# Performance work log

Hardware: AMD Instinct MI355X
Metric: run time of the kernel (lower is better)

## Reference

```python
import jax, jax.numpy as jnp
import numpy as np

DIM = 320
HEADS = 8
D_HEAD = 40
CTX_DIM = 768
INNER_FF = 4 * DIM  # 1280
EPS = 1e-5


def _ln(x, w, b):
    mu = jnp.mean(x, axis=-1, keepdims=True)
    var = jnp.mean(jnp.square(x - mu), axis=-1, keepdims=True)
    return (x - mu) * jax.lax.rsqrt(var + EPS) * w + b


def _attn(xq, ctx, Wq, Wk, Wv, Wo, bo):
    # Wq: [dim, inner]; Wk/Wv: [ctx_dim, inner]; Wo: [inner, dim]
    b, n, _ = xq.shape
    m = ctx.shape[1]
    scale = D_HEAD ** -0.5
    q = (xq @ Wq).reshape(b, n, HEADS, D_HEAD)
    k = (ctx @ Wk).reshape(b, m, HEADS, D_HEAD)
    v = (ctx @ Wv).reshape(b, m, HEADS, D_HEAD)
    sim = jnp.einsum('bihd,bjhd->bhij', q, k) * scale
    attn = jax.nn.softmax(sim, axis=-1)
    out = jnp.einsum('bhij,bjhd->bihd', attn, v).reshape(b, n, HEADS * D_HEAD)
    return out @ Wo + bo


def setup_inputs() -> dict:
    key = jax.random.key(0)
    ks = jax.random.split(key, 20)
    s = 0.02
    inner = HEADS * D_HEAD  # 320
    d = {
        'x': jax.random.normal(ks[0], (2, 4096, DIM), jnp.float32),
        'context': jax.random.normal(ks[1], (2, 77, CTX_DIM), jnp.float32),
        # norm params
        'ln1_w': jnp.ones((DIM,)), 'ln1_b': jnp.zeros((DIM,)),
        'ln2_w': jnp.ones((DIM,)), 'ln2_b': jnp.zeros((DIM,)),
        'ln3_w': jnp.ones((DIM,)), 'ln3_b': jnp.zeros((DIM,)),
        # attn1 (self)
        'a1_Wq': jax.random.normal(ks[2], (DIM, inner)) * s,
        'a1_Wk': jax.random.normal(ks[3], (DIM, inner)) * s,
        'a1_Wv': jax.random.normal(ks[4], (DIM, inner)) * s,
        'a1_Wo': jax.random.normal(ks[5], (inner, DIM)) * s,
        'a1_bo': jnp.zeros((DIM,)),
        # attn2 (cross)
        'a2_Wq': jax.random.normal(ks[6], (DIM, inner)) * s,
        'a2_Wk': jax.random.normal(ks[7], (CTX_DIM, inner)) * s,
        'a2_Wv': jax.random.normal(ks[8], (CTX_DIM, inner)) * s,
        'a2_Wo': jax.random.normal(ks[9], (inner, DIM)) * s,
        'a2_bo': jnp.zeros((DIM,)),
        # GEGLU feed-forward
        'ff_W1': jax.random.normal(ks[10], (DIM, 2 * INNER_FF)) * s,
        'ff_b1': jnp.zeros((2 * INNER_FF,)),
        'ff_W2': jax.random.normal(ks[11], (INNER_FF, DIM)) * s,
        'ff_b2': jnp.zeros((DIM,)),
    }
    return d


def reference(x, context, ln1_w, ln1_b, ln2_w, ln2_b, ln3_w, ln3_b,
              a1_Wq, a1_Wk, a1_Wv, a1_Wo, a1_bo,
              a2_Wq, a2_Wk, a2_Wv, a2_Wo, a2_bo,
              ff_W1, ff_b1, ff_W2, ff_b2):
    h = _ln(x, ln1_w, ln1_b)
    x = _attn(h, h, a1_Wq, a1_Wk, a1_Wv, a1_Wo, a1_bo) + x
    h = _ln(x, ln2_w, ln2_b)
    x = _attn(h, context, a2_Wq, a2_Wk, a2_Wv, a2_Wo, a2_bo) + x
    h = _ln(x, ln3_w, ln3_b)
    proj = h @ ff_W1 + ff_b1
    u, gate = jnp.split(proj, 2, axis=-1)
    ff = (u * jax.nn.gelu(gate, approximate=False)) @ ff_W2 + ff_b2
    return ff + x
```

## Files before the change

kernel.cpp:

```cpp
#include <hip/hip_runtime.h>
#include <hip/hip_bf16.h>
#include <math.h>

typedef __hip_bfloat16 bf16;
typedef __attribute__((ext_vector_type(8))) short bf16x8;
typedef __attribute__((ext_vector_type(4))) short bf16x4;
typedef __attribute__((ext_vector_type(4))) float f32x4;
typedef __attribute__((ext_vector_type(2))) unsigned int u32x2;

#define DIM 320
#define HEADS 8
#define DHEAD 40
#define CTXD 768
#define FFI 1280
#define NQ 4096
#define NCTX 77
#define BATCH 2

static __device__ __forceinline__ short f2bs(float v) {
    union { bf16 b; short s; } x; x.b = __float2bfloat16(v); return x.s;
}
static __device__ __forceinline__ float bs2f(short s) {
    return __uint_as_float(((unsigned)(unsigned short)s) << 16);
}
// ... 60 lines not shown
            for (int j = 0; j < 8; ++j) { v[j] = rp[j]; s += v[j]; s2 += v[j] * v[j]; }
        }
    }
#pragma unroll
    for (int off = 32; off; off >>= 1) { s += __shfl_xor(s, off); s2 += __shfl_xor(s2, off); }
    float mean = s * (1.f / DIM);
    float var = s2 * (1.f / DIM) - mean * mean;
    float rstd = rsqrtf(var + 1e-5f);
    if (lane < 40) {
        bf16x8 ov;
#pragma unroll
        for (int j = 0; j < 8; ++j)
            ov[j] = f2bs((v[j] - mean) * rstd * w[lane * 8 + j] + bp[lane * 8 + j]);
        *(bf16x8*)(out + (size_t)row * DIM + lane * 8) = ov;
    }
}

template<int MODE>
__global__ void __launch_bounds__(256) gemm128(const short* __restrict__ A,
                          const short* __restrict__ Wt,
                          const float* __restrict__ bias,
                          const float* __restrict__ res,
                          short* __restrict__ resb,
                          short* __restrict__ outb,
                          float* __restrict__ outf,
                          int N, int K, float oscale)
{
    __shared__ short As[128 * 72];
    __shared__ short Bs[64 * 72];
    const int tid = threadIdx.x;
    const int w = tid >> 6, lane = tid & 63, lrow = lane & 15, lgrp = lane >> 4;
    const int wr = w >> 1, wc = w & 1;
    const int m0 = blockIdx.y * 128, n0 = blockIdx.x * 64;
    f32x4 acc[4][2] = {};
    for (int k0 = 0; k0 < K; k0 += 64) {
        __syncthreads();
#pragma unroll
        for (int l = 0; l < 4; ++l) {
            int idx = tid + (l << 8);
            int arow = idx >> 3, ac = idx & 7;
            *(bf16x8*)&As[arow * 72 + ac * 8] =
                *(const bf16x8*)(A + (size_t)(m0 + arow) * K + k0 + ac * 8);
        }
#pragma unroll
        for (int l = 0; l < 2; ++l) {
            int idx = tid + (l << 8);
            int brow = idx >> 3, bc = idx & 7;
            *(bf16x8*)&Bs[brow * 72 + bc * 8] =
                *(const bf16x8*)(Wt + (size_t)(n0 + brow) * K + k0 + bc * 8);
        }
        __syncthreads();
#pragma unroll
        for (int s = 0; s < 2; ++s) {
            bf16x8 b0 = *(const bf16x8*)&Bs[(wc * 32 + lrow) * 72 + s * 32 + lgrp * 8];
            bf16x8 b1 = *(const bf16x8*)&Bs[(wc * 32 + 16 + lrow) * 72 + s * 32 + lgrp * 8];
#pragma unroll
            for (int m = 0; m < 4; ++m) {
                bf16x8 a = *(const bf16x8*)&As[(wr * 64 + m * 16 + lrow) * 72 + s * 32 + lgrp * 8];
                acc[m][0] = __builtin_amdgcn_mfma_f32_16x16x32_bf16(a, b0, acc[m][0], 0, 0, 0);
                acc[m][1] = __builtin_amdgcn_mfma_f32_16x16x32_bf16(a, b1, acc[m][1], 0, 0, 0);
            }
        }
    }
#pragma unroll
    for (int n = 0; n < 2; ++n) {
        int col = n0 + wc * 32 + n * 16 + lrow;
        float bvx = bias ? bias[col] : 0.f;
#pragma unroll
        for (int m = 0; m < 4; ++m) {
#pragma unroll
            for (int r = 0; r < 4; ++r) {
                int row = m0 + wr * 64 + m * 16 + lgrp * 4 + r;
                float v = acc[m][n][r] + bvx;
                size_t o = (size_t)row * N + col;
                if (MODE == 0)      outb[o] = f2bs(v * oscale);
                else if (MODE == 1) resb[o] = f2bs(v + res[o]);
                else if (MODE == 2) resb[o] = f2bs(v + bs2f(resb[o]));
                else                outf[o] = v + bs2f(resb[o]);
            }
        }
    }
}

__global__ void __launch_bounds__(256) qkv128(const short* __restrict__ A,
                          const short* __restrict__ wq, const short* __restrict__ wk,
                          const short* __restrict__ wv,
                          short* __restrict__ qb, short* __restrict__ kbuf,
                          short* __restrict__ vts, float qscale)
{
    __shared__ short As[128 * 72];
    __shared__ short Bs[64 * 72];
    const int tid = threadIdx.x;
    const int z = blockIdx.z;
    const short* Wt = z == 0 ? wq : z == 1 ? wk : wv;
    const int w = tid >> 6, lane = tid & 63, lrow = lane & 15, lgrp = lane >> 4;
    const int wr = w >> 1, wc = w & 1;
    const int m0 = blockIdx.y * 128, n0 = blockIdx.x * 64;
    f32x4 acc[4][2] = {};
    for (int k0 = 0; k0 < DIM; k0 += 64) {
        __syncthreads();
#pragma unroll
        for (int l = 0; l < 4; ++l) {
            int idx = tid + (l << 8);
            int arow = idx >> 3, ac = idx & 7;
            *(bf16x8*)&As[arow * 72 + ac * 8] =
                *(const bf16x8*)(A + (size_t)(m0 + arow) * DIM + k0 + ac * 8);
        }
#pragma unroll
        for (int l = 0; l < 2; ++l) {
            int idx = tid + (l << 8);
            int brow = idx >> 3, bc = idx & 7;
            *(bf16x8*)&Bs[brow * 72 + bc * 8] =
                *(const bf16x8*)(Wt + (size_t)(n0 + brow) * DIM + k0 + bc * 8);
        }
        __syncthreads();
#pragma unroll
        for (int s = 0; s < 2; ++s) {
            bf16x8 b0 = *(const bf16x8*)&Bs[(wc * 32 + lrow) * 72 + s * 32 + lgrp * 8];
            bf16x8 b1 = *(const bf16x8*)&Bs[(wc * 32 + 16 + lrow) * 72 + s * 32 + lgrp * 8];
#pragma unroll
            for (int m = 0; m < 4; ++m) {
                bf16x8 a = *(const bf16x8*)&As[(wr * 64 + m * 16 + lrow) * 72 + s * 32 + lgrp * 8];
                acc[m][0] = __builtin_amdgcn_mfma_f32_16x16x32_bf16(a, b0, acc[m][0], 0, 0, 0);
                acc[m][1] = __builtin_amdgcn_mfma_f32_16x16x32_bf16(a, b1, acc[m][1], 0, 0, 0);
            }
        }
    }
#pragma unroll
    for (int n = 0; n < 2; ++n) {
        int col = n0 + wc * 32 + n * 16 + lrow;
#pragma unroll
        for (int m = 0; m < 4; ++m) {
            if (z == 2) {
                int row0 = m0 + wr * 64 + m * 16 + lgrp * 4;
                int b_ = row0 >> 12, kv = row0 & (NQ - 1);
                int hh = col / DHEAD, d = col - hh * DHEAD;
                bf16x4 pv;
#pragma unroll
                for (int r = 0; r < 4; ++r) pv[r] = f2bs(acc[m][n][r]);
                *(bf16x4*)(vts + (size_t)((b_ * HEADS + hh) * 48 + d) * NQ + kv) = pv;
            } else {
#pragma unroll
                for (int r = 0; r < 4; ++r) {
                    int row = m0 + wr * 64 + m * 16 + lgrp * 4 + r;
                    float v = acc[m][n][r];
                    if (z == 0) qb[(size_t)row * DIM + col] = f2bs(v * qscale);
                    else        kbuf[(size_t)row * DIM + col] = f2bs(v);
                }
            }
        }
    }
}

__global__ void __launch_bounds__(256) geglu128(const short* __restrict__ A,
                           const short* __restrict__ Wt1,
                           const float* __restrict__ b1, short* __restrict__ G)
{
    __shared__ short As[128 * 72];
    __shared__ short Bu[64 * 72];
    __shared__ short Bg[64 * 72];
    const int tid = threadIdx.x;
    const int w = tid >> 6, lane = tid & 63, lrow = lane & 15, lgrp = lane >> 4;
    const int wr = w >> 1, wc = w & 1;
    const int m0 = blockIdx.y * 128, n0 = blockIdx.x * 64;
    f32x4 au[4][2] = {}, ag[4][2] = {};
    for (int k0 = 0; k0 < DIM; k0 += 64) {
        __syncthreads();
#pragma unroll
        for (int l = 0; l < 4; ++l) {
            int idx = tid + (l << 8);
            int arow = idx >> 3, ac = idx & 7;
            *(bf16x8*)&As[arow * 72 + ac * 8] =
                *(const bf16x8*)(A + (size_t)(m0 + arow) * DIM + k0 + ac * 8);
        }
#pragma unroll
        for (int l = 0; l < 2; ++l) {
            int idx = tid + (l << 8);
            int brow = idx >> 3, bc = idx & 7;
            *(bf16x8*)&Bu[brow * 72 + bc * 8] =
                *(const bf16x8*)(Wt1 + (size_t)(n0 + brow) * DIM + k0 + bc * 8);
            *(bf16x8*)&Bg[brow * 72 + bc * 8] =
                *(const bf16x8*)(Wt1 + (size_t)(FFI + n0 + brow) * DIM + k0 + bc * 8);
        }
        __syncthreads();
#pragma unroll
        for (int s = 0; s < 2; ++s) {
            bf16x8 bu0 = *(const bf16x8*)&Bu[(wc * 32 + lrow) * 72 + s * 32 + lgrp * 8];
            bf16x8 bu1 = *(const bf16x8*)&Bu[(wc * 32 + 16 + lrow) * 72 + s * 32 + lgrp * 8];
            bf16x8 bg0 = *(const bf16x8*)&Bg[(wc * 32 + lrow) * 72 + s * 32 + lgrp * 8];
            bf16x8 bg1 = *(const bf16x8*)&Bg[(wc * 32 + 16 + lrow) * 72 + s * 32 + lgrp * 8];
#pragma unroll
            for (int m = 0; m < 4; ++m) {
                bf16x8 a = *(const bf16x8*)&As[(wr * 64 + m * 16 + lrow) * 72 + s * 32 + lgrp * 8];
                au[m][0] = __builtin_amdgcn_mfma_f32_16x16x32_bf16(a, bu0, au[m][0], 0, 0, 0);
                au[m][1] = __builtin_amdgcn_mfma_f32_16x16x32_bf16(a, bu1, au[m][1], 0, 0, 0);
                ag[m][0] = __builtin_amdgcn_mfma_f32_16x16x32_bf16(a, bg0, ag[m][0], 0, 0, 0);
                ag[m][1] = __builtin_amdgcn_mfma_f32_16x16x32_bf16(a, bg1, ag[m][1], 0, 0, 0);
            }
        }
    }
#pragma unroll
    for (int n = 0; n < 2; ++n) {
        int col = n0 + wc * 32 + n * 16 + lrow;
        float bu = b1[col], bg = b1[FFI + col];
#pragma unroll
        for (int m = 0; m < 4; ++m) {
#pragma unroll
            for (int r = 0; r < 4; ++r) {
                int row = m0 + wr * 64 + m * 16 + lgrp * 4 + r;
                float u = au[m][n][r] + bu;
                float g = ag[m][n][r] + bg;
                float gelu = 0.5f * g * (1.f + erff(g * 0.70710678f));
                G[(size_t)row * FFI + col] = f2bs(u * gelu);
            }
        }
    }
}

__global__ void __launch_bounds__(256) mfma_crosskv(const float* __restrict__ ctx,
                          const short* __restrict__ wk2, const short* __restrict__ wv2,
                          short* __restrict__ k2, short* __restrict__ vt2)
{
    __shared__ short As[64 * 72];
    __shared__ short Bs[64 * 72];
    const int tid = threadIdx.x;
    const int z = blockIdx.z;
    const short* Wt = z ? wv2 : wk2;
    const int Mc = BATCH * NCTX;
    const int w = tid >> 6, lane = tid & 63, lrow = lane & 15, lgrp = lane >> 4;
    const int m0 = blockIdx.y * 64, n0 = blockIdx.x * 64;
    f32x4 acc[4] = {};
    for (int kb = 0; kb < CTXD / 64; ++kb) {
        const int k0 = kb << 6;
        __syncthreads();
#pragma unroll
        for (int l = 0; l < 2; ++l) {
            int idx = tid + (l << 8);
            int arow = idx >> 3, ac = idx & 7;
            int grow = m0 + arow;
            bf16x8 v = {};
            if (grow < Mc) {
                const float* Af = ctx + (size_t)grow * CTXD + k0 + ac * 8;
#pragma unroll
                for (int j = 0; j < 8; ++j) v[j] = f2bs(Af[j]);
            }
            *(bf16x8*)&As[arow * 72 + ac * 8] = v;
            *(bf16x8*)&Bs[arow * 72 + ac * 8] =
                *(const bf16x8*)(Wt + (size_t)(n0 + arow) * CTXD + k0 + ac * 8);
        }
        __syncthreads();
#pragma unroll
        for (int s = 0; s < 2; ++s) {
            bf16x8 a = *(const bf16x8*)&As[(w * 16 + lrow) * 72 + s * 32 + lgrp * 8];
#pragma unroll
            for (int ct = 0; ct < 4; ++ct) {
                bf16x8 b = *(const bf16x8*)&Bs[(ct * 16 + lrow) * 72 + s * 32 + lgrp * 8];
                acc[ct] = __builtin_amdgcn_mfma_f32_16x16x32_bf16(a, b, acc[ct], 0, 0, 0);
            }
        }
    }
#pragma unroll
    for (int ct = 0; ct < 4; ++ct) {
        int col = n0 + ct * 16 + lrow;
#pragma unroll
        for (int r = 0; r < 4; ++r) {
            int row = m0 + w * 16 + lgrp * 4 + r;
            if (row >= Mc) continue;
            float v = acc[ct][r];
            if (z == 0) k2[(size_t)row * DIM + col] = f2bs(v);
            else {
                int b_ = row / NCTX, kv = row - b_ * NCTX;
                int hh = col / DHEAD, d = col - hh * DHEAD;
                vt2[(size_t)((b_ * HEADS + hh) * 48 + d) * 128 + kv] = f2bs(v);
            }
        }
    }
}

template<bool FULL>
__global__ void __launch_bounds__(256) flash_mfma(const short* __restrict__ Q,
                           const short* __restrict__ Kb,
                           const short* __restrict__ VtG,
                           short* __restrict__ O,
                           int kvlen, int kvs)
{
    __shared__ short Ks[2][64 * 64];
    __shared__ short Vt[2][48 * 64];
    __shared__ short Ps[128 * 64];
    const int tid = threadIdx.x;
    const int w = tid >> 6, lane = tid & 63, lrow = lane & 15, lgrp = lane >> 4;
    const int hh = blockIdx.y, b = blockIdx.z;
    const int q0 = blockIdx.x * 128;
    const int swz = (lrow & 7) << 4;

    for (int i = tid; i < 1024; i += 256) ((bf16x8*)Ks)[i] = (bf16x8){};
    for (int i = tid; i < 768; i += 256) {
        short fill = (((i % 384) >> 3) == 40) ? (short)0x3F80 : (short)0;
        bf16x8 f8 = {fill, fill, fill, fill, fill, fill, fill, fill};
        ((bf16x8*)Vt)[i] = f8;
    }

    const size_t qra = (size_t)(b * NQ + q0 + w * 32 + lrow) * DIM + hh * DHEAD;
    const size_t qrb = qra + (size_t)16 * DIM;
    bf16x8 bq0a = *(const bf16x8*)(Q + qra + lgrp * 8);
    bf16x8 bq0b = *(const bf16x8*)(Q + qrb + lgrp * 8);
    bf16x8 bq1a = {}, bq1b = {};
    if (lgrp == 0) {
        bq1a = *(const bf16x8*)(Q + qra + 32);
        bq1b = *(const bf16x8*)(Q + qrb + 32);
    }

    const int kv0 = tid / 5, cc0 = tid % 5;
    const bool isK1 = tid < 64;
    const int kv1 = (256 + tid) / 5, cc1 = (256 + tid) % 5;
    const int vd1 = (tid - 64) >> 3, vcc1 = (tid - 64) & 7;
    const bool hasV2 = tid < 128;
    const int vd2 = (192 + tid) >> 3, vcc2 = (192 + tid) & 7;

    bf16x8 st0, st1, st2;
    const size_t kbase = (size_t)b * kvlen;
    const size_t vbase = (size_t)((b * HEADS + hh) * 48);

    auto issue = [&](int t) {
        const int j0 = t << 6;
        st0 = *(const bf16x8*)(Kb + (kbase + j0 + kv0) * DIM + hh * DHEAD + cc0 * 8);
        if (isK1) st1 = *(const bf16x8*)(Kb + (kbase + j0 + kv1) * DIM + hh * DHEAD + cc1 * 8);
        else      st1 = *(const bf16x8*)(VtG + (vbase + vd1) * kvs + j0 + vcc1 * 8);
        if (hasV2) st2 = *(const bf16x8*)(VtG + (vbase + vd2) * kvs + j0 + vcc2 * 8);
    };
    auto commit = [&](int bi) {
        *(bf16x8*)((char*)Ks[bi] + kv0 * 128 + ((cc0 * 16) ^ ((kv0 & 7) << 4))) = st0;
        if (isK1)
            *(bf16x8*)((char*)Ks[bi] + kv1 * 128 + ((cc1 * 16) ^ ((kv1 & 7) << 4))) = st1;
        else
            *(bf16x8*)((char*)Vt[bi] + vd1 * 128 + ((vcc1 * 16) ^ ((vd1 & 7) << 4))) = st1;
        if (hasV2)
            *(bf16x8*)((char*)Vt[bi] + vd2 * 128 + ((vcc2 * 16) ^ ((vd2 & 7) << 4))) = st2;
    };

    f32x4 oa[3] = {}, ob[3] = {};

    issue(0);
    __syncthreads();
    commit(0);
    const int ntiles = (kvlen + 63) >> 6;
    char* prow_a = (char*)Ps + (w * 32 + lrow) * 128;
    char* prow_b = prow_a + 16 * 128;
    for (int t = 0; t < ntiles; ++t) {
        const int j0 = t << 6;
        const int bi = t & 1;
        if (t + 1 < ntiles) issue(t + 1);
        __syncthreads();

        f32x4 sa[4] = {}, sb[4] = {};
        __builtin_amdgcn_s_setprio(1);
#pragma unroll
        for (int ct = 0; ct < 4; ++ct) {
            const char* krow = (char*)Ks[bi] + (ct * 16 + lrow) * 128;
            bf16x8 ak0 = *(const bf16x8*)(krow + ((lgrp * 16) ^ swz));
            bf16x8 ak1 = *(const bf16x8*)(krow + ((64 + lgrp * 16) ^ swz));
            sa[ct] = __builtin_amdgcn_mfma_f32_16x16x32_bf16(ak0, bq0a, sa[ct], 0, 0, 0);
            sb[ct] = __builtin_amdgcn_mfma_f32_16x16x32_bf16(ak0, bq0b, sb[ct], 0, 0, 0);
            sa[ct] = __builtin_amdgcn_mfma_f32_16x16x32_bf16(ak1, bq1a, sa[ct], 0, 0, 0);
            sb[ct] = __builtin_amdgcn_mfma_f32_16x16x32_bf16(ak1, bq1b, sb[ct], 0, 0, 0);
        }
        __builtin_amdgcn_s_setprio(0);
        if (!FULL && j0 + 64 > kvlen) {
#pragma unroll
            for (int ct = 0; ct < 4; ++ct)
#pragma unroll
                for (int r = 0; r < 4; ++r)
                    if (j0 + ct * 16 + lgrp * 4 + r >= kvlen) { sa[ct][r] = -1e30f; sb[ct][r] = -1e30f; }
        }
#pragma unroll
        for (int ct = 0; ct < 4; ++ct) {
            float a0 = __builtin_amdgcn_exp2f(sa[ct][0]);
            float a1 = __builtin_amdgcn_exp2f(sa[ct][1]);
            float a2 = __builtin_amdgcn_exp2f(sa[ct][2]);
            float a3 = __builtin_amdgcn_exp2f(sa[ct][3]);
            u32x2 pka; pka[0] = pkbf(a1, a0); pka[1] = pkbf(a3, a2);
            *(u32x2*)(prow_a + ((ct * 32 + lgrp * 8) ^ swz)) = pka;
            float b0 = __builtin_amdgcn_exp2f(sb[ct][0]);
            float b1 = __builtin_amdgcn_exp2f(sb[ct][1]);
            float b2 = __builtin_amdgcn_exp2f(sb[ct][2]);
            float b3 = __builtin_amdgcn_exp2f(sb[ct][3]);
            u32x2 pkb; pkb[0] = pkbf(b1, b0); pkb[1] = pkbf(b3, b2);
            *(u32x2*)(prow_b + ((ct * 32 + lgrp * 8) ^ swz)) = pkb;
        }
        __builtin_amdgcn_s_setprio(1);
#pragma unroll
        for (int s = 0; s < 2; ++s) {
            bf16x8 bpa = *(const bf16x8*)(prow_a + ((s * 64 + lgrp * 16) ^ swz));
            bf16x8 bpb = *(const bf16x8*)(prow_b + ((s * 64 + lgrp * 16) ^ swz));
#pragma unroll
            for (int dt = 0; dt < 3; ++dt) {
                bf16x8 av = *(const bf16x8*)((char*)Vt[bi] + (dt * 16 + lrow) * 128 + ((s * 64 + lgrp * 16) ^ swz));
                oa[dt] = __builtin_amdgcn_mfma_f32_16x16x32_bf16(av, bpa, oa[dt], 0, 0, 0);
                ob[dt] = __builtin_amdgcn_mfma_f32_16x16x32_bf16(av, bpb, ob[dt], 0, 0, 0);
            }
        }
        __builtin_amdgcn_s_setprio(0);
        if (t + 1 < ntiles) commit((t + 1) & 1);
    }
    float la = __shfl(oa[2][0], 32 + lrow);
    float lb = __shfl(ob[2][0], 32 + lrow);
    float ia = 1.f / la, ib = 1.f / lb;
#pragma unroll
    for (int dt = 0; dt < 3; ++dt) {
        int dbase = dt * 16 + lgrp * 4;
        if (dbase < DHEAD) {
            u32x2 ova, ovb;
            ova[0] = pkbf(oa[dt][1] * ia, oa[dt][0] * ia);
            ova[1] = pkbf(oa[dt][3] * ia, oa[dt][2] * ia);
            *(u32x2*)(O + qra + dbase) = ova;
            ovb[0] = pkbf(ob[dt][1] * ib, ob[dt][0] * ib);
            ovb[1] = pkbf(ob[dt][3] * ib, ob[dt][2] * ib);
            *(u32x2*)(O + qrb + dbase) = ovb;
        }
    }
}

extern "C" void kernel_launch(void* const* d_in, const int* in_sizes, int n_in,
                              void* d_out, int out_size, void* d_ws, size_t ws_size,
                              hipStream_t stream)
{
    const float* x      = (const float*)d_in[0];
    const float* ctx    = (const float*)d_in[1];
    const float* ln1_w  = (const float*)d_in[2];
    const float* ln1_b  = (const float*)d_in[3];
    const float* ln2_w  = (const float*)d_in[4];
    const float* ln2_b  = (const float*)d_in[5];
    const float* ln3_w  = (const float*)d_in[6];
    const float* ln3_b  = (const float*)d_in[7];
    const float* a1_Wq  = (const float*)d_in[8];
    const float* a1_Wk  = (const float*)d_in[9];
    const float* a1_Wv  = (const float*)d_in[10];
    const float* a1_Wo  = (const float*)d_in[11];
    const float* a1_bo  = (const float*)d_in[12];
    const float* a2_Wq  = (const float*)d_in[13];
    const float* a2_Wk  = (const float*)d_in[14];
    const float* a2_Wv  = (const float*)d_in[15];
    const float* a2_Wo  = (const float*)d_in[16];
    const float* a2_bo  = (const float*)d_in[17];
    const float* ff_W1  = (const float*)d_in[18];
    const float* ff_b1  = (const float*)d_in[19];
    const float* ff_W2  = (const float*)d_in[20];
    const float* ff_b2  = (const float*)d_in[21];

    const int M = BATCH * NQ;
    const float qscale2 = (float)(0.15811388300841898 * 1.4426950408889634);

    char* p = (char*)d_ws;
    auto carve = [&](size_t bytes) { char* r = p; p += (bytes + 255) & ~255ULL; return r; };
    short* h       = (short*)carve((size_t)M * DIM * 2);
    short* qb      = (short*)carve((size_t)M * DIM * 2);
    short* kbuf    = (short*)carve((size_t)M * DIM * 2);
    short* attnout = (short*)carve((size_t)M * DIM * 2);
    short* resb    = (short*)carve((size_t)M * DIM * 2);
    short* gbuf    = (short*)carve((size_t)M * FFI * 2);
    short* VtS     = (short*)carve((size_t)BATCH * HEADS * 48 * NQ * 2);
    short* Vt2     = (short*)carve((size_t)BATCH * HEADS * 48 * 128 * 2);
    short* k2      = (short*)carve((size_t)256 * DIM * 2);
    short* wtq1    = (short*)carve((size_t)DIM * DIM * 2);
    short* wtk1    = (short*)carve((size_t)DIM * DIM * 2);
    short* wtv1    = (short*)carve((size_t)DIM * DIM * 2);
    short* wto1    = (short*)carve((size_t)DIM * DIM * 2);
    short* wtq2    = (short*)carve((size_t)DIM * DIM * 2);
    short* wto2    = (short*)carve((size_t)DIM * DIM * 2);
    short* wtk2    = (short*)carve((size_t)DIM * CTXD * 2);
    short* wtv2    = (short*)carve((size_t)DIM * CTXD * 2);
    short* wt1     = (short*)carve((size_t)2 * FFI * DIM * 2);
    short* wt2     = (short*)carve((size_t)DIM * FFI * 2);

    dim3 blk(256);
    dim3 g128(DIM / 64, M / 128);
    dim3 gattn(NQ / 128, HEADS, BATCH);

    wtrans_all<<<2280, blk, 0, stream>>>(a1_Wq, a1_Wk, a1_Wv, a1_Wo, a2_Wq, a2_Wo,
                                         a2_Wk, a2_Wv, ff_W1, ff_W2,
                                         wtq1, wtk1, wtv1, wto1, wtq2, wto2,
                                         wtk2, wtv2, wt1, wt2);
    ln_kernel<false><<<M / 4, blk, 0, stream>>>(x, ln1_w, ln1_b, h, M);
    qkv128<<<dim3(5, 64, 3), blk, 0, stream>>>(h, wtq1, wtk1, wtv1, qb, kbuf, VtS, qscale2);
    flash_mfma<true><<<gattn, blk, 0, stream>>>(qb, kbuf, VtS, attnout, NQ, NQ);
    gemm128<1><<<g128, blk, 0, stream>>>(attnout, wto1, a1_bo, x, resb, nullptr, nullptr, DIM, DIM, 1.f);
    ln_kernel<true><<<M / 4, blk, 0, stream>>>(resb, ln2_w, ln2_b, h, M);
    gemm128<0><<<g128, blk, 0, stream>>>(h, wtq2, nullptr, nullptr, nullptr, qb, nullptr, DIM, DIM, qscale2);
    mfma_crosskv<<<dim3(5, 3, 2), blk, 0, stream>>>(ctx, wtk2, wtv2, k2, Vt2);
    flash_mfma<false><<<gattn, blk, 0, stream>>>(qb, k2, Vt2, attnout, NCTX, 128);
    gemm128<2><<<g128, blk, 0, stream>>>(attnout, wto2, a2_bo, nullptr, resb, nullptr, nullptr, DIM, DIM, 1.f);
    ln_kernel<true><<<M / 4, blk, 0, stream>>>(resb, ln3_w, ln3_b, h, M);
    geglu128<<<dim3(FFI / 64, M / 128), blk, 0, stream>>>(h, wt1, ff_b1, gbuf);
    gemm128<3><<<g128, blk, 0, stream>>>(gbuf, wt2, ff_b2, nullptr, resb, nullptr, (float*)d_out, DIM, FFI, 1.f);
}
```

Measured before the change: 233.9 us.

## Fuse Q/K/V and cross K/V projections; restructure flash attention prefetch loop

The self-attention QKV projection now computes Q, K and V in one block that shares the loaded activation tile, instead of three grid slices that each reload it. The cross-attention K/V projection is fused the same way. The flash attention loop is unrolled by two with fixed double-buffer indices, precomputed swizzled shared-memory offsets and incremented global pointers, and it now commits the prefetched tile at the top of each iteration. In exchange, the QKV kernel holds three times the accumulators and launches a third as many blocks, which may lower occupancy. The prefetch also reads past the end of the K/V data, so the k2 buffer is enlarged to absorb those over-reads.

```diff
diff --git a/kernel.cpp b/kernel.cpp
--- a/kernel.cpp
+++ b/kernel.cpp
@@ -166,21 +166,21 @@
     }
 }
 
-__global__ void __launch_bounds__(256) qkv128(const short* __restrict__ A,
+__global__ void __launch_bounds__(256) qkv_fused(const short* __restrict__ A,
                           const short* __restrict__ wq, const short* __restrict__ wk,
                           const short* __restrict__ wv,
                           short* __restrict__ qb, short* __restrict__ kbuf,
                           short* __restrict__ vts, float qscale)
 {
     __shared__ short As[128 * 72];
-    __shared__ short Bs[64 * 72];
+    __shared__ short Bq[64 * 72];
+    __shared__ short Bk[64 * 72];
+    __shared__ short Bv[64 * 72];
     const int tid = threadIdx.x;
-    const int z = blockIdx.z;
-    const short* Wt = z == 0 ? wq : z == 1 ? wk : wv;
     const int w = tid >> 6, lane = tid & 63, lrow = lane & 15, lgrp = lane >> 4;
     const int wr = w >> 1, wc = w & 1;
     const int m0 = blockIdx.y * 128, n0 = blockIdx.x * 64;
-    f32x4 acc[4][2] = {};
+    f32x4 aq[4][2] = {}, ak[4][2] = {}, av[4][2] = {};
     for (int k0 = 0; k0 < DIM; k0 += 64) {
         __syncthreads();
 #pragma unroll
@@ -194,44 +194,109 @@
         for (int l = 0; l < 2; ++l) {
             int idx = tid + (l << 8);
             int brow = idx >> 3, bc = idx & 7;
-            *(bf16x8*)&Bs[brow * 72 + bc * 8] =
-                *(const bf16x8*)(Wt + (size_t)(n0 + brow) * DIM + k0 + bc * 8);
+            size_t wo = (size_t)(n0 + brow) * DIM + k0 + bc * 8;
+            *(bf16x8*)&Bq[brow * 72 + bc * 8] = *(const bf16x8*)(wq + wo);
+            *(bf16x8*)&Bk[brow * 72 + bc * 8] = *(const bf16x8*)(wk + wo);
+            *(bf16x8*)&Bv[brow * 72 + bc * 8] = *(const bf16x8*)(wv + wo);
         }
         __syncthreads();
 #pragma unroll
         for (int s = 0; s < 2; ++s) {
-            bf16x8 b0 = *(const bf16x8*)&Bs[(wc * 32 + lrow) * 72 + s * 32 + lgrp * 8];
-            bf16x8 b1 = *(const bf16x8*)&Bs[(wc * 32 + 16 + lrow) * 72 + s * 32 + lgrp * 8];
+            int bo0 = (wc * 32 + lrow) * 72 + s * 32 + lgrp * 8;
+            int bo1 = bo0 + 16 * 72;
+            bf16x8 q0 = *(const bf16x8*)&Bq[bo0], q1 = *(const bf16x8*)&Bq[bo1];
+            bf16x8 kk0 = *(const bf16x8*)&Bk[bo0], kk1 = *(const bf16x8*)&Bk[bo1];
+            bf16x8 v0 = *(const bf16x8*)&Bv[bo0], v1 = *(const bf16x8*)&Bv[bo1];
 #pragma unroll
             for (int m = 0; m < 4; ++m) {
                 bf16x8 a = *(const bf16x8*)&As[(wr * 64 + m * 16 + lrow) * 72 + s * 32 + lgrp * 8];
-                acc[m][0] = __builtin_amdgcn_mfma_f32_16x16x32_bf16(a, b0, acc[m][0], 0, 0, 0);
-                acc[m][1] = __builtin_amdgcn_mfma_f32_16x16x32_bf16(a, b1, acc[m][1], 0, 0, 0);
+                aq[m][0] = __builtin_amdgcn_mfma_f32_16x16x32_bf16(a, q0, aq[m][0], 0, 0, 0);
+                aq[m][1] = __builtin_amdgcn_mfma_f32_16x16x32_bf16(a, q1, aq[m][1], 0, 0, 0);
+                ak[m][0] = __builtin_amdgcn_mfma_f32_16x16x32_bf16(a, kk0, ak[m][0], 0, 0, 0);
+                ak[m][1] = __builtin_amdgcn_mfma_f32_16x16x32_bf16(a, kk1, ak[m][1], 0, 0, 0);
+                av[m][0] = __builtin_amdgcn_mfma_f32_16x16x32_bf16(a, v0, av[m][0], 0, 0, 0);
+                av[m][1] = __builtin_amdgcn_mfma_f32_16x16x32_bf16(a, v1, av[m][1], 0, 0, 0);
             }
         }
     }
 #pragma unroll
     for (int n = 0; n < 2; ++n) {
         int col = n0 + wc * 32 + n * 16 + lrow;
+        int hh = col / DHEAD, d = col - hh * DHEAD;
 #pragma unroll
         for (int m = 0; m < 4; ++m) {
-            if (z == 2) {
-                int row0 = m0 + wr * 64 + m * 16 + lgrp * 4;
-                int b_ = row0 >> 12, kv = row0 & (NQ - 1);
-                int hh = col / DHEAD, d = col - hh * DHEAD;
-                bf16x4 pv;
-#pragma unroll
-                for (int r = 0; r < 4; ++r) pv[r] = f2bs(acc[m][n][r]);
-                *(bf16x4*)(vts + (size_t)((b_ * HEADS + hh) * 48 + d) * NQ + kv) = pv;
-            } else {
-#pragma unroll
-                for (int r = 0; r < 4; ++r) {
-                    int row = m0 + wr * 64 + m * 16 + lgrp * 4 + r;
-                    float v = acc[m][n][r];
-                    if (z == 0) qb[(size_t)row * DIM + col] = f2bs(v * qscale);
-                    else        kbuf[(size_t)row * DIM + col] = f2bs(v);
-                }
-            }
+            int row0 = m0 + wr * 64 + m * 16 + lgrp * 4;
+            int b_ = row0 >> 12, kv = row0 & (NQ - 1);
+            bf16x4 pv;
+#pragma unroll
+            for (int r = 0; r < 4; ++r) pv[r] = f2bs(av[m][n][r]);
+            *(bf16x4*)(vts + (size_t)((b_ * HEADS + hh) * 48 + d) * NQ + kv) = pv;
+#pragma unroll
+            for (int r = 0; r < 4; ++r) {
+                int row = row0 + r;
+                qb[(size_t)row * DIM + col] = f2bs(aq[m][n][r] * qscale);
+                kbuf[(size_t)row * DIM + col] = f2bs(ak[m][n][r]);
+            }
+        }
+    }
+}
+
+__global__ void __launch_bounds__(256) crosskv_fused(const float* __restrict__ ctx,
+                          const short* __restrict__ wk2, const short* __restrict__ wv2,
+                          short* __restrict__ k2, short* __restrict__ vt2)
+{
+    __shared__ short As[64 * 72];
+    __shared__ short Bk[64 * 72];
+    __shared__ short Bv[64 * 72];
+    const int tid = threadIdx.x;
+    const int Mc = BATCH * NCTX;
+    const int w = tid >> 6, lane = tid & 63, lrow = lane & 15, lgrp = lane >> 4;
+    const int m0 = blockIdx.y * 64, n0 = blockIdx.x * 64;
+    f32x4 acck[4] = {}, accv[4] = {};
+    for (int kb = 0; kb < CTXD / 64; ++kb) {
+        const int k0 = kb << 6;
+        __syncthreads();
+#pragma unroll
+        for (int l = 0; l < 2; ++l) {
+            int idx = tid + (l << 8);
+            int arow = idx >> 3, ac = idx & 7;
+            int grow = m0 + arow;
+            bf16x8 v = {};
+            if (grow < Mc) {
+                const float* Af = ctx + (size_t)grow * CTXD + k0 + ac * 8;
+#pragma unroll
+                for (int j = 0; j < 8; ++j) v[j] = f2bs(Af[j]);
+            }
+            *(bf16x8*)&As[arow * 72 + ac * 8] = v;
+            size_t wo = (size_t)(n0 + arow) * CTXD + k0 + ac * 8;
+            *(bf16x8*)&Bk[arow * 72 + ac * 8] = *(const bf16x8*)(wk2 + wo);
+            *(bf16x8*)&Bv[arow * 72 + ac * 8] = *(const bf16x8*)(wv2 + wo);
+        }
+        __syncthreads();
+#pragma unroll
+        for (int s = 0; s < 2; ++s) {
+            bf16x8 a = *(const bf16x8*)&As[(w * 16 + lrow) * 72 + s * 32 + lgrp * 8];
+#pragma unroll
+            for (int ct = 0; ct < 4; ++ct) {
+                int bo = (ct * 16 + lrow) * 72 + s * 32 + lgrp * 8;
+                bf16x8 bk = *(const bf16x8*)&Bk[bo];
+                acck[ct] = __builtin_amdgcn_mfma_f32_16x16x32_bf16(a, bk, acck[ct], 0, 0, 0);
+                bf16x8 bv = *(const bf16x8*)&Bv[bo];
+                accv[ct] = __builtin_amdgcn_mfma_f32_16x16x32_bf16(a, bv, accv[ct], 0, 0, 0);
+            }
+        }
+    }
+#pragma unroll
+    for (int ct = 0; ct < 4; ++ct) {
+        int col = n0 + ct * 16 + lrow;
+        int hh = col / DHEAD, d = col - hh * DHEAD;
+#pragma unroll
+        for (int r = 0; r < 4; ++r) {
+            int row = m0 + w * 16 + lgrp * 4 + r;
+            if (row >= Mc) continue;
+            k2[(size_t)row * DIM + col] = f2bs(acck[ct][r]);
+            int b_ = row / NCTX, kv = row - b_ * NCTX;
+            vt2[(size_t)((b_ * HEADS + hh) * 48 + d) * 128 + kv] = f2bs(accv[ct][r]);
         }
     }
 }
@@ -301,66 +366,6 @@
     }
 }
 
-__global__ void __launch_bounds__(256) mfma_crosskv(const float* __restrict__ ctx,
-                          const short* __restrict__ wk2, const short* __restrict__ wv2,
-                          short* __restrict__ k2, short* __restrict__ vt2)
-{
-    __shared__ short As[64 * 72];
-    __shared__ short Bs[64 * 72];
-    const int tid = threadIdx.x;
-    const int z = blockIdx.z;
-    const short* Wt = z ? wv2 : wk2;
-    const int Mc = BATCH * NCTX;
-    const int w = tid >> 6, lane = tid & 63, lrow = lane & 15, lgrp = lane >> 4;
-    const int m0 = blockIdx.y * 64, n0 = blockIdx.x * 64;
-    f32x4 acc[4] = {};
-    for (int kb = 0; kb < CTXD / 64; ++kb) {
-        const int k0 = kb << 6;
-        __syncthreads();
-#pragma unroll
-        for (int l = 0; l < 2; ++l) {
-            int idx = tid + (l << 8);
-            int arow = idx >> 3, ac = idx & 7;
-            int grow = m0 + arow;
-            bf16x8 v = {};
-            if (grow < Mc) {
-                const float* Af = ctx + (size_t)grow * CTXD + k0 + ac * 8;
-#pragma unroll
-                for (int j = 0; j < 8; ++j) v[j] = f2bs(Af[j]);
-            }
-            *(bf16x8*)&As[arow * 72 + ac * 8] = v;
-            *(bf16x8*)&Bs[arow * 72 + ac * 8] =
-                *(const bf16x8*)(Wt + (size_t)(n0 + arow) * CTXD + k0 + ac * 8);
-        }
-        __syncthreads();
-#pragma unroll
-        for (int s = 0; s < 2; ++s) {
-            bf16x8 a = *(const bf16x8*)&As[(w * 16 + lrow) * 72 + s * 32 + lgrp * 8];
-#pragma unroll
-            for (int ct = 0; ct < 4; ++ct) {
-                bf16x8 b = *(const bf16x8*)&Bs[(ct * 16 + lrow) * 72 + s * 32 + lgrp * 8];
-                acc[ct] = __builtin_amdgcn_mfma_f32_16x16x32_bf16(a, b, acc[ct], 0, 0, 0);
-            }
-        }
-    }
-#pragma unroll
-    for (int ct = 0; ct < 4; ++ct) {
-        int col = n0 + ct * 16 + lrow;
-#pragma unroll
-        for (int r = 0; r < 4; ++r) {
-            int row = m0 + w * 16 + lgrp * 4 + r;
-            if (row >= Mc) continue;
-            float v = acc[ct][r];
-            if (z == 0) k2[(size_t)row * DIM + col] = f2bs(v);
-            else {
-                int b_ = row / NCTX, kv = row - b_ * NCTX;
-                int hh = col / DHEAD, d = col - hh * DHEAD;
-                vt2[(size_t)((b_ * HEADS + hh) * 48 + d) * 128 + kv] = f2bs(v);
-            }
-        }
-    }
-}
-
 template<bool FULL>
 __global__ void __launch_bounds__(256) flash_mfma(const short* __restrict__ Q,
                            const short* __restrict__ Kb,
@@ -401,40 +406,41 @@
     const bool hasV2 = tid < 128;
     const int vd2 = (192 + tid) >> 3, vcc2 = (192 + tid) & 7;
 
-    bf16x8 st0, st1, st2;
     const size_t kbase = (size_t)b * kvlen;
     const size_t vbase = (size_t)((b * HEADS + hh) * 48);
 
-    auto issue = [&](int t) {
-        const int j0 = t << 6;
-        st0 = *(const bf16x8*)(Kb + (kbase + j0 + kv0) * DIM + hh * DHEAD + cc0 * 8);
-        if (isK1) st1 = *(const bf16x8*)(Kb + (kbase + j0 + kv1) * DIM + hh * DHEAD + cc1 * 8);
-        else      st1 = *(const bf16x8*)(VtG + (vbase + vd1) * kvs + j0 + vcc1 * 8);
-        if (hasV2) st2 = *(const bf16x8*)(VtG + (vbase + vd2) * kvs + j0 + vcc2 * 8);
+    const short* kp0 = Kb + (kbase + kv0) * DIM + hh * DHEAD + cc0 * 8;
+    const short* kp1 = Kb + (kbase + (isK1 ? kv1 : 0)) * DIM + hh * DHEAD + (isK1 ? cc1 : 0) * 8;
+    const short* vp1 = VtG + (vbase + (isK1 ? 0 : vd1)) * kvs + (isK1 ? 0 : vcc1) * 8;
+    const short* vp2 = VtG + (vbase + (hasV2 ? vd2 : 0)) * kvs + (hasV2 ? vcc2 : 0) * 8;
+
+    const int koff0 = kv0 * 128 + ((cc0 * 16) ^ ((kv0 & 7) << 4));
+    const int koff1 = kv1 * 128 + ((cc1 * 16) ^ ((kv1 & 7) << 4));
+    const int voff1 = vd1 * 128 + ((vcc1 * 16) ^ ((vd1 & 7) << 4));
+    const int voff2 = vd2 * 128 + ((vcc2 * 16) ^ ((vd2 & 7) << 4));
+
+    bf16x8 st0, st1, st2;
+    auto issue = [&]() {
+        st0 = *(const bf16x8*)kp0; kp0 += 64 * DIM;
+        if (isK1) { st1 = *(const bf16x8*)kp1; kp1 += 64 * DIM; }
+        else      { st1 = *(const bf16x8*)vp1; vp1 += 64; }
+        if (hasV2) { st2 = *(const bf16x8*)vp2; vp2 += 64; }
     };
     auto commit = [&](int bi) {
-        *(bf16x8*)((char*)Ks[bi] + kv0 * 128 + ((cc0 * 16) ^ ((kv0 & 7) << 4))) = st0;
-        if (isK1)
-            *(bf16x8*)((char*)Ks[bi] + kv1 * 128 + ((cc1 * 16) ^ ((kv1 & 7) << 4))) = st1;
-        else
-            *(bf16x8*)((char*)Vt[bi] + vd1 * 128 + ((vcc1 * 16) ^ ((vd1 & 7) << 4))) = st1;
-        if (hasV2)
-            *(bf16x8*)((char*)Vt[bi] + vd2 * 128 + ((vcc2 * 16) ^ ((vd2 & 7) << 4))) = st2;
+        *(bf16x8*)((char*)Ks[bi] + koff0) = st0;
+        if (isK1)  *(bf16x8*)((char*)Ks[bi] + koff1) = st1;
+        else       *(bf16x8*)((char*)Vt[bi] + voff1) = st1;
+        if (hasV2) *(bf16x8*)((char*)Vt[bi] + voff2) = st2;
     };
 
     f32x4 oa[3] = {}, ob[3] = {};
-
-    issue(0);
-    __syncthreads();
-    commit(0);
-    const int ntiles = (kvlen + 63) >> 6;
     char* prow_a = (char*)Ps + (w * 32 + lrow) * 128;
     char* prow_b = prow_a + 16 * 128;
-    for (int t = 0; t < ntiles; ++t) {
-        const int j0 = t << 6;
-        const int bi = t & 1;
-        if (t + 1 < ntiles) issue(t + 1);
-        __syncthreads();
+
+    auto body = [&](int t, int bi) {
+        __syncthreads();
+        commit(bi ^ 1);
+        issue();
 
         f32x4 sa[4] = {}, sb[4] = {};
         __builtin_amdgcn_s_setprio(1);
@@ -449,12 +455,12 @@
             sb[ct] = __builtin_amdgcn_mfma_f32_16x16x32_bf16(ak1, bq1b, sb[ct], 0, 0, 0);
         }
         __builtin_amdgcn_s_setprio(0);
-        if (!FULL && j0 + 64 > kvlen) {
+        if (!FULL && (t << 6) + 64 > kvlen) {
 #pragma unroll
             for (int ct = 0; ct < 4; ++ct)
 #pragma unroll
                 for (int r = 0; r < 4; ++r)
-                    if (j0 + ct * 16 + lgrp * 4 + r >= kvlen) { sa[ct][r] = -1e30f; sb[ct][r] = -1e30f; }
+                    if ((t << 6) + ct * 16 + lgrp * 4 + r >= kvlen) { sa[ct][r] = -1e30f; sb[ct][r] = -1e30f; }
         }
 #pragma unroll
         for (int ct = 0; ct < 4; ++ct) {
@@ -484,8 +490,18 @@
             }
         }
         __builtin_amdgcn_s_setprio(0);
-        if (t + 1 < ntiles) commit((t + 1) & 1);
-    }
+    };
+
+    issue();
+    __syncthreads();
+    commit(0);
+    issue();
+    const int ntiles = (kvlen + 63) >> 6;
+    for (int t = 0; t < ntiles; t += 2) {
+        body(t, 0);
+        body(t + 1, 1);
+    }
+
     float la = __shfl(oa[2][0], 32 + lrow);
     float lb = __shfl(ob[2][0], 32 + lrow);
     float ia = 1.f / la, ib = 1.f / lb;
@@ -544,7 +560,7 @@
     short* gbuf    = (short*)carve((size_t)M * FFI * 2);
     short* VtS     = (short*)carve((size_t)BATCH * HEADS * 48 * NQ * 2);
     short* Vt2     = (short*)carve((size_t)BATCH * HEADS * 48 * 128 * 2);
-    short* k2      = (short*)carve((size_t)256 * DIM * 2);
+    short* k2      = (short*)carve((size_t)512 * DIM * 2);
     short* wtq1    = (short*)carve((size_t)DIM * DIM * 2);
     short* wtk1    = (short*)carve((size_t)DIM * DIM * 2);
     short* wtv1    = (short*)carve((size_t)DIM * DIM * 2);
@@ -565,12 +581,12 @@
                                          wtq1, wtk1, wtv1, wto1, wtq2, wto2,
                                          wtk2, wtv2, wt1, wt2);
     ln_kernel<false><<<M / 4, blk, 0, stream>>>(x, ln1_w, ln1_b, h, M);
-    qkv128<<<dim3(5, 64, 3), blk, 0, stream>>>(h, wtq1, wtk1, wtv1, qb, kbuf, VtS, qscale2);
+    qkv_fused<<<g128, blk, 0, stream>>>(h, wtq1, wtk1, wtv1, qb, kbuf, VtS, qscale2);
     flash_mfma<true><<<gattn, blk, 0, stream>>>(qb, kbuf, VtS, attnout, NQ, NQ);
     gemm128<1><<<g128, blk, 0, stream>>>(attnout, wto1, a1_bo, x, resb, nullptr, nullptr, DIM, DIM, 1.f);
     ln_kernel<true><<<M / 4, blk, 0, stream>>>(resb, ln2_w, ln2_b, h, M);
     gemm128<0><<<g128, blk, 0, stream>>>(h, wtq2, nullptr, nullptr, nullptr, qb, nullptr, DIM, DIM, qscale2);
-    mfma_crosskv<<<dim3(5, 3, 2), blk, 0, stream>>>(ctx, wtk2, wtv2, k2, Vt2);
+    crosskv_fused<<<dim3(5, 3), blk, 0, stream>>>(ctx, wtk2, wtv2, k2, Vt2);
     flash_mfma<false><<<gattn, blk, 0, stream>>>(qb, k2, Vt2, attnout, NCTX, 128);
     gemm128<2><<<g128, blk, 0, stream>>>(attnout, wto2, a2_bo, nullptr, resb, nullptr, nullptr, DIM, DIM, 1.f);
     ln_kernel<true><<<M / 4, blk, 0, stream>>>(resb, ln3_w, ln3_b, h, M);
```

Measured after the change: 244.4 us. 1.04x slower.

## Software-pipeline flash attention: defer PV matmul one tile and triple-buffer V

Applied to the files above, without the earlier changes.

Restructures the flash attention loop so the P·V MFMA for tile t-1 runs while tile t's QK scores and exponentials are computed. P gets double buffers and V triple buffers so the next tile's global-to-LDS commit can happen right after the barrier. Global load pointers and LDS offsets are precomputed and advanced incrementally, and prefetching now runs two tiles ahead, which over-reads past kvlen (hence the enlarged k2 buffer). The cost is more LDS per block, which may lower occupancy, and one extra drain step after the loop.

```diff
diff --git a/kernel.cpp b/kernel.cpp
--- a/kernel.cpp
+++ b/kernel.cpp
@@ -236,71 +236,6 @@
     }
 }
 
-__global__ void __launch_bounds__(256) geglu128(const short* __restrict__ A,
-                           const short* __restrict__ Wt1,
-                           const float* __restrict__ b1, short* __restrict__ G)
-{
-    __shared__ short As[128 * 72];
-    __shared__ short Bu[64 * 72];
-    __shared__ short Bg[64 * 72];
-    const int tid = threadIdx.x;
-    const int w = tid >> 6, lane = tid & 63, lrow = lane & 15, lgrp = lane >> 4;
-    const int wr = w >> 1, wc = w & 1;
-    const int m0 = blockIdx.y * 128, n0 = blockIdx.x * 64;
-    f32x4 au[4][2] = {}, ag[4][2] = {};
-    for (int k0 = 0; k0 < DIM; k0 += 64) {
-        __syncthreads();
-#pragma unroll
-        for (int l = 0; l < 4; ++l) {
-            int idx = tid + (l << 8);
-            int arow = idx >> 3, ac = idx & 7;
-            *(bf16x8*)&As[arow * 72 + ac * 8] =
-                *(const bf16x8*)(A + (size_t)(m0 + arow) * DIM + k0 + ac * 8);
-        }
-#pragma unroll
-        for (int l = 0; l < 2; ++l) {
-            int idx = tid + (l << 8);
-            int brow = idx >> 3, bc = idx & 7;
-            *(bf16x8*)&Bu[brow * 72 + bc * 8] =
-                *(const bf16x8*)(Wt1 + (size_t)(n0 + brow) * DIM + k0 + bc * 8);
-            *(bf16x8*)&Bg[brow * 72 + bc * 8] =
-                *(const bf16x8*)(Wt1 + (size_t)(FFI + n0 + brow) * DIM + k0 + bc * 8);
-        }
-        __syncthreads();
-#pragma unroll
-        for (int s = 0; s < 2; ++s) {
-            bf16x8 bu0 = *(const bf16x8*)&Bu[(wc * 32 + lrow) * 72 + s * 32 + lgrp * 8];
-            bf16x8 bu1 = *(const bf16x8*)&Bu[(wc * 32 + 16 + lrow) * 72 + s * 32 + lgrp * 8];
-            bf16x8 bg0 = *(const bf16x8*)&Bg[(wc * 32 + lrow) * 72 + s * 32 + lgrp * 8];
-            bf16x8 bg1 = *(const bf16x8*)&Bg[(wc * 32 + 16 + lrow) * 72 + s * 32 + lgrp * 8];
-#pragma unroll
-            for (int m = 0; m < 4; ++m) {
-                bf16x8 a = *(const bf16x8*)&As[(wr * 64 + m * 16 + lrow) * 72 + s * 32 + lgrp * 8];
-                au[m][0] = __builtin_amdgcn_mfma_f32_16x16x32_bf16(a, bu0, au[m][0], 0, 0, 0);
-                au[m][1] = __builtin_amdgcn_mfma_f32_16x16x32_bf16(a, bu1, au[m][1], 0, 0, 0);
-                ag[m][0] = __builtin_amdgcn_mfma_f32_16x16x32_bf16(a, bg0, ag[m][0], 0, 0, 0);
-                ag[m][1] = __builtin_amdgcn_mfma_f32_16x16x32_bf16(a, bg1, ag[m][1], 0, 0, 0);
-            }
-        }
-    }
-#pragma unroll
-    for (int n = 0; n < 2; ++n) {
-        int col = n0 + wc * 32 + n * 16 + lrow;
-        float bu = b1[col], bg = b1[FFI + col];
-#pragma unroll
-        for (int m = 0; m < 4; ++m) {
-#pragma unroll
-            for (int r = 0; r < 4; ++r) {
-                int row = m0 + wr * 64 + m * 16 + lgrp * 4 + r;
-                float u = au[m][n][r] + bu;
-                float g = ag[m][n][r] + bg;
-                float gelu = 0.5f * g * (1.f + erff(g * 0.70710678f));
-                G[(size_t)row * FFI + col] = f2bs(u * gelu);
-            }
-        }
-    }
-}
-
 __global__ void __launch_bounds__(256) mfma_crosskv(const float* __restrict__ ctx,
                           const short* __restrict__ wk2, const short* __restrict__ wv2,
                           short* __restrict__ k2, short* __restrict__ vt2)
@@ -361,6 +296,71 @@
     }
 }
 
+__global__ void __launch_bounds__(256) geglu128(const short* __restrict__ A,
+                           const short* __restrict__ Wt1,
+                           const float* __restrict__ b1, short* __restrict__ G)
+{
+    __shared__ short As[128 * 72];
+    __shared__ short Bu[64 * 72];
+    __shared__ short Bg[64 * 72];
+    const int tid = threadIdx.x;
+    const int w = tid >> 6, lane = tid & 63, lrow = lane & 15, lgrp = lane >> 4;
+    const int wr = w >> 1, wc = w & 1;
+    const int m0 = blockIdx.y * 128, n0 = blockIdx.x * 64;
+    f32x4 au[4][2] = {}, ag[4][2] = {};
+    for (int k0 = 0; k0 < DIM; k0 += 64) {
+        __syncthreads();
+#pragma unroll
+        for (int l = 0; l < 4; ++l) {
+            int idx = tid + (l << 8);
+            int arow = idx >> 3, ac = idx & 7;
+            *(bf16x8*)&As[arow * 72 + ac * 8] =
+                *(const bf16x8*)(A + (size_t)(m0 + arow) * DIM + k0 + ac * 8);
+        }
+#pragma unroll
+        for (int l = 0; l < 2; ++l) {
+            int idx = tid + (l << 8);
+            int brow = idx >> 3, bc = idx & 7;
+            *(bf16x8*)&Bu[brow * 72 + bc * 8] =
+                *(const bf16x8*)(Wt1 + (size_t)(n0 + brow) * DIM + k0 + bc * 8);
+            *(bf16x8*)&Bg[brow * 72 + bc * 8] =
+                *(const bf16x8*)(Wt1 + (size_t)(FFI + n0 + brow) * DIM + k0 + bc * 8);
+        }
+        __syncthreads();
+#pragma unroll
+        for (int s = 0; s < 2; ++s) {
+            bf16x8 bu0 = *(const bf16x8*)&Bu[(wc * 32 + lrow) * 72 + s * 32 + lgrp * 8];
+            bf16x8 bu1 = *(const bf16x8*)&Bu[(wc * 32 + 16 + lrow) * 72 + s * 32 + lgrp * 8];
+            bf16x8 bg0 = *(const bf16x8*)&Bg[(wc * 32 + lrow) * 72 + s * 32 + lgrp * 8];
+            bf16x8 bg1 = *(const bf16x8*)&Bg[(wc * 32 + 16 + lrow) * 72 + s * 32 + lgrp * 8];
+#pragma unroll
+            for (int m = 0; m < 4; ++m) {
+                bf16x8 a = *(const bf16x8*)&As[(wr * 64 + m * 16 + lrow) * 72 + s * 32 + lgrp * 8];
+                au[m][0] = __builtin_amdgcn_mfma_f32_16x16x32_bf16(a, bu0, au[m][0], 0, 0, 0);
+                au[m][1] = __builtin_amdgcn_mfma_f32_16x16x32_bf16(a, bu1, au[m][1], 0, 0, 0);
+                ag[m][0] = __builtin_amdgcn_mfma_f32_16x16x32_bf16(a, bg0, ag[m][0], 0, 0, 0);
+                ag[m][1] = __builtin_amdgcn_mfma_f32_16x16x32_bf16(a, bg1, ag[m][1], 0, 0, 0);
+            }
+        }
+    }
+#pragma unroll
+    for (int n = 0; n < 2; ++n) {
+        int col = n0 + wc * 32 + n * 16 + lrow;
+        float bu = b1[col], bg = b1[FFI + col];
+#pragma unroll
+        for (int m = 0; m < 4; ++m) {
+#pragma unroll
+            for (int r = 0; r < 4; ++r) {
+                int row = m0 + wr * 64 + m * 16 + lgrp * 4 + r;
+                float u = au[m][n][r] + bu;
+                float g = ag[m][n][r] + bg;
+                float gelu = 0.5f * g * (1.f + erff(g * 0.70710678f));
+                G[(size_t)row * FFI + col] = f2bs(u * gelu);
+            }
+        }
+    }
+}
+
 template<bool FULL>
 __global__ void __launch_bounds__(256) flash_mfma(const short* __restrict__ Q,
                            const short* __restrict__ Kb,
@@ -369,8 +369,8 @@
                            int kvlen, int kvs)
 {
     __shared__ short Ks[2][64 * 64];
-    __shared__ short Vt[2][48 * 64];
-    __shared__ short Ps[128 * 64];
+    __shared__ short Vt[3][48 * 64];
+    __shared__ short Ps[2][128 * 64];
     const int tid = threadIdx.x;
     const int w = tid >> 6, lane = tid & 63, lrow = lane & 15, lgrp = lane >> 4;
     const int hh = blockIdx.y, b = blockIdx.z;
@@ -378,7 +378,7 @@
     const int swz = (lrow & 7) << 4;
 
     for (int i = tid; i < 1024; i += 256) ((bf16x8*)Ks)[i] = (bf16x8){};
-    for (int i = tid; i < 768; i += 256) {
+    for (int i = tid; i < 1152; i += 256) {
         short fill = (((i % 384) >> 3) == 40) ? (short)0x3F80 : (short)0;
         bf16x8 f8 = {fill, fill, fill, fill, fill, fill, fill, fill};
         ((bf16x8*)Vt)[i] = f8;
@@ -401,46 +401,78 @@
     const bool hasV2 = tid < 128;
     const int vd2 = (192 + tid) >> 3, vcc2 = (192 + tid) & 7;
 
-    bf16x8 st0, st1, st2;
     const size_t kbase = (size_t)b * kvlen;
     const size_t vbase = (size_t)((b * HEADS + hh) * 48);
 
-    auto issue = [&](int t) {
-        const int j0 = t << 6;
-        st0 = *(const bf16x8*)(Kb + (kbase + j0 + kv0) * DIM + hh * DHEAD + cc0 * 8);
-        if (isK1) st1 = *(const bf16x8*)(Kb + (kbase + j0 + kv1) * DIM + hh * DHEAD + cc1 * 8);
-        else      st1 = *(const bf16x8*)(VtG + (vbase + vd1) * kvs + j0 + vcc1 * 8);
-        if (hasV2) st2 = *(const bf16x8*)(VtG + (vbase + vd2) * kvs + j0 + vcc2 * 8);
+    const short* kp0 = Kb + (kbase + kv0) * DIM + hh * DHEAD + cc0 * 8;
+    const short* kp1 = Kb + (kbase + (isK1 ? kv1 : 0)) * DIM + hh * DHEAD + (isK1 ? cc1 : 0) * 8;
+    const short* vp1 = VtG + (vbase + (isK1 ? 0 : vd1)) * kvs + (isK1 ? 0 : vcc1) * 8;
+    const short* vp2 = VtG + (vbase + (hasV2 ? vd2 : 0)) * kvs + (hasV2 ? vcc2 : 0) * 8;
+
+    const int koff0 = kv0 * 128 + ((cc0 * 16) ^ ((kv0 & 7) << 4));
+    const int koff1 = kv1 * 128 + ((cc1 * 16) ^ ((kv1 & 7) << 4));
+    const int voff1 = vd1 * 128 + ((vcc1 * 16) ^ ((vd1 & 7) << 4));
+    const int voff2 = vd2 * 128 + ((vcc2 * 16) ^ ((vd2 & 7) << 4));
+
+    bf16x8 st0, st1, st2;
+    auto issue = [&]() {
+        st0 = *(const bf16x8*)kp0; kp0 += 64 * DIM;
+        if (isK1) { st1 = *(const bf16x8*)kp1; kp1 += 64 * DIM; }
+        else      { st1 = *(const bf16x8*)vp1; vp1 += 64; }
+        if (hasV2) { st2 = *(const bf16x8*)vp2; vp2 += 64; }
     };
-    auto commit = [&](int bi) {
-        *(bf16x8*)((char*)Ks[bi] + kv0 * 128 + ((cc0 * 16) ^ ((kv0 & 7) << 4))) = st0;
-        if (isK1)
-            *(bf16x8*)((char*)Ks[bi] + kv1 * 128 + ((cc1 * 16) ^ ((kv1 & 7) << 4))) = st1;
-        else
-            *(bf16x8*)((char*)Vt[bi] + vd1 * 128 + ((vcc1 * 16) ^ ((vd1 & 7) << 4))) = st1;
-        if (hasV2)
-            *(bf16x8*)((char*)Vt[bi] + vd2 * 128 + ((vcc2 * 16) ^ ((vd2 & 7) << 4))) = st2;
+    auto commit = [&](char* kb_, char* vb_) {
+        *(bf16x8*)(kb_ + koff0) = st0;
+        if (isK1)  *(bf16x8*)(kb_ + koff1) = st1;
+        else       *(bf16x8*)(vb_ + voff1) = st1;
+        if (hasV2) *(bf16x8*)(vb_ + voff2) = st2;
     };
 
     f32x4 oa[3] = {}, ob[3] = {};
 
-    issue(0);
+    char* kcur = (char*)Ks[0];
+    char* knxt = (char*)Ks[1];
+    char* vprev = (char*)Vt[2];
+    char* vcur  = (char*)Vt[0];
+    char* vnxt  = (char*)Vt[1];
+    const int prow_off = (w * 32 + lrow) * 128;
+    char* pcur  = (char*)Ps[0] + prow_off;
+    char* pprev = (char*)Ps[1] + prow_off;
+
+    auto pv_step = [&](char* vb_, char* pb_) {
+        __builtin_amdgcn_s_setprio(1);
+#pragma unroll
+        for (int s = 0; s < 2; ++s) {
+            bf16x8 bpa = *(const bf16x8*)(pb_ + ((s * 64 + lgrp * 16) ^ swz));
+            bf16x8 bpb = *(const bf16x8*)(pb_ + 2048 + ((s * 64 + lgrp * 16) ^ swz));
+#pragma unroll
+            for (int dt = 0; dt < 3; ++dt) {
+                bf16x8 av = *(const bf16x8*)(vb_ + (dt * 16 + lrow) * 128 + ((s * 64 + lgrp * 16) ^ swz));
+                oa[dt] = __builtin_amdgcn_mfma_f32_16x16x32_bf16(av, bpa, oa[dt], 0, 0, 0);
+                ob[dt] = __builtin_amdgcn_mfma_f32_16x16x32_bf16(av, bpb, ob[dt], 0, 0, 0);
+            }
+        }
+        __builtin_amdgcn_s_setprio(0);
+    };
+
+    issue();
     __syncthreads();
-    commit(0);
+    commit(kcur, vcur);
+    issue();
+
     const int ntiles = (kvlen + 63) >> 6;
-    char* prow_a = (char*)Ps + (w * 32 + lrow) * 128;
-    char* prow_b = prow_a + 16 * 128;
     for (int t = 0; t < ntiles; ++t) {
-        const int j0 = t << 6;
-        const int bi = t & 1;
-        if (t + 1 < ntiles) issue(t + 1);
-        __syncthreads();
+        __syncthreads();
+        commit(knxt, vnxt);
+        issue();
+
+        if (t > 0) pv_step(vprev, pprev);
 
         f32x4 sa[4] = {}, sb[4] = {};
         __builtin_amdgcn_s_setprio(1);
 #pragma unroll
         for (int ct = 0; ct < 4; ++ct) {
-            const char* krow = (char*)Ks[bi] + (ct * 16 + lrow) * 128;
+            const char* krow = kcur + (ct * 16 + lrow) * 128;
             bf16x8 ak0 = *(const bf16x8*)(krow + ((lgrp * 16) ^ swz));
             bf16x8 ak1 = *(const bf16x8*)(krow + ((64 + lgrp * 16) ^ swz));
             sa[ct] = __builtin_amdgcn_mfma_f32_16x16x32_bf16(ak0, bq0a, sa[ct], 0, 0, 0);
@@ -449,12 +481,12 @@
             sb[ct] = __builtin_amdgcn_mfma_f32_16x16x32_bf16(ak1, bq1b, sb[ct], 0, 0, 0);
         }
         __builtin_amdgcn_s_setprio(0);
-        if (!FULL && j0 + 64 > kvlen) {
+        if (!FULL && (t << 6) + 64 > kvlen) {
 #pragma unroll
             for (int ct = 0; ct < 4; ++ct)
 #pragma unroll
                 for (int r = 0; r < 4; ++r)
-                    if (j0 + ct * 16 + lgrp * 4 + r >= kvlen) { sa[ct][r] = -1e30f; sb[ct][r] = -1e30f; }
+                    if ((t << 6) + ct * 16 + lgrp * 4 + r >= kvlen) { sa[ct][r] = -1e30f; sb[ct][r] = -1e30f; }
         }
 #pragma unroll
         for (int ct = 0; ct < 4; ++ct) {
@@ -463,29 +495,20 @@
             float a2 = __builtin_amdgcn_exp2f(sa[ct][2]);
             float a3 = __builtin_amdgcn_exp2f(sa[ct][3]);
             u32x2 pka; pka[0] = pkbf(a1, a0); pka[1] = pkbf(a3, a2);
-            *(u32x2*)(prow_a + ((ct * 32 + lgrp * 8) ^ swz)) = pka;
+            *(u32x2*)(pcur + ((ct * 32 + lgrp * 8) ^ swz)) = pka;
             float b0 = __builtin_amdgcn_exp2f(sb[ct][0]);
             float b1 = __builtin_amdgcn_exp2f(sb[ct][1]);
             float b2 = __builtin_amdgcn_exp2f(sb[ct][2]);
             float b3 = __builtin_amdgcn_exp2f(sb[ct][3]);
             u32x2 pkb; pkb[0] = pkbf(b1, b0); pkb[1] = pkbf(b3, b2);
-            *(u32x2*)(prow_b + ((ct * 32 + lgrp * 8) ^ swz)) = pkb;
-        }
-        __builtin_amdgcn_s_setprio(1);
-#pragma unroll
-        for (int s = 0; s < 2; ++s) {
-            bf16x8 bpa = *(const bf16x8*)(prow_a + ((s * 64 + lgrp * 16) ^ swz));
-            bf16x8 bpb = *(const bf16x8*)(prow_b + ((s * 64 + lgrp * 16) ^ swz));
-#pragma unroll
-            for (int dt = 0; dt < 3; ++dt) {
-                bf16x8 av = *(const bf16x8*)((char*)Vt[bi] + (dt * 16 + lrow) * 128 + ((s * 64 + lgrp * 16) ^ swz));
-                oa[dt] = __builtin_amdgcn_mfma_f32_16x16x32_bf16(av, bpa, oa[dt], 0, 0, 0);
-                ob[dt] = __builtin_amdgcn_mfma_f32_16x16x32_bf16(av, bpb, ob[dt], 0, 0, 0);
-            }
-        }
-        __builtin_amdgcn_s_setprio(0);
-        if (t + 1 < ntiles) commit((t + 1) & 1);
-    }
+            *(u32x2*)(pcur + 2048 + ((ct * 32 + lgrp * 8) ^ swz)) = pkb;
+        }
+        { char* tk = kcur; kcur = knxt; knxt = tk; }
+        { char* tv = vprev; vprev = vcur; vcur = vnxt; vnxt = tv; }
+        { char* tp = pprev; pprev = pcur; pcur = tp; }
+    }
+    pv_step(vprev, pprev);
+
     float la = __shfl(oa[2][0], 32 + lrow);
     float lb = __shfl(ob[2][0], 32 + lrow);
     float ia = 1.f / la, ib = 1.f / lb;
@@ -544,7 +567,7 @@
     short* gbuf    = (short*)carve((size_t)M * FFI * 2);
     short* VtS     = (short*)carve((size_t)BATCH * HEADS * 48 * NQ * 2);
     short* Vt2     = (short*)carve((size_t)BATCH * HEADS * 48 * 128 * 2);
-    short* k2      = (short*)carve((size_t)256 * DIM * 2);
+    short* k2      = (short*)carve((size_t)512 * DIM * 2);
     short* wtq1    = (short*)carve((size_t)DIM * DIM * 2);
     short* wtk1    = (short*)carve((size_t)DIM * DIM * 2);
     short* wtv1    = (short*)carve((size_t)DIM * DIM * 2);
```

Measured after the change: 232.5 us. About the same (-0.6%).
